# Kernel optimization log

Measured on AMD Instinct MI355X. Metric: run time of the kernel, lower is better.

Reference implementation:

```python
import jax, jax.numpy as jnp
import numpy as np

TOP_P = 0.9  # forward default arg, fixed to exercise the top-p path


def setup_inputs() -> dict:
    key = jax.random.key(0)
    k1, k2 = jax.random.split(key)
    B, V = 128, 128000
    logits = jax.random.normal(k1, (B, V), dtype=jnp.float32) * 2.0
    # temperatures in [0.5, 1.5) to avoid divide-by-near-zero
    temperatures = jax.random.uniform(k2, (B,), dtype=jnp.float32, minval=0.5, maxval=1.5)
    return {"logits": logits, "temperatures": temperatures, "top_k": 50}


def reference(logits, temperatures, top_k):
    B, V = logits.shape
    neg_inf = jnp.float32(-jnp.inf)

    # temperature scale + softmax
    scaled = logits.astype(jnp.float32) / temperatures[:, None]
    probs = jax.nn.softmax(scaled, axis=-1)  # (B, V)

    brow = jnp.arange(B)[:, None]

    # top-k filter: keep top-k probs, fill rest with -inf (matches torch scatter into full(-inf))
    if top_k > 0:
        k = min(top_k, V)
        vals, idx = jax.lax.top_k(probs, k)  # (B, k)
        probs = jnp.full_like(probs, neg_inf).at[brow, idx].set(vals)

    # top-p (nucleus) filter: sort desc, cumsum, mask tail beyond top_p (always keep first)
    if TOP_P < 1.0:
        order = jnp.argsort(-probs, axis=-1)              # descending order indices (-inf sorts last)
        sorted_probs = jnp.take_along_axis(probs, order, axis=-1)
        cum = jnp.cumsum(sorted_probs, axis=-1)
        remove = cum > TOP_P
        remove = remove.at[:, 0].set(False)
        sorted_probs = jnp.where(remove, neg_inf, sorted_probs)
        probs = probs.at[brow, order].set(sorted_probs)   # scatter back to original positions

    # Gumbel-max-style sampling: argmax(probs / Exp(1) noise), noise clamped to >= 1e-10
    kn = jax.random.fold_in(jax.random.key(0), 1)
    noise = jnp.maximum(jax.random.exponential(kn, probs.shape, dtype=jnp.float32), 1e-10)
    return jnp.argmax(probs / noise, axis=-1)  # (B,) int tokens
```

## Files before the change

kernel.cpp:

```cpp
#include <hip/hip_runtime.h>
#include <stdint.h>
#include <limits.h>

#define THREEFRY_PARTITIONABLE 1

#define NTK   512
#define NWAVE (NTK/64)
#define RCAP  4
#define NBUCK 4096
#define BPT   (NBUCK/NTK)
#define CAPS  256
#define CAPG  2048
#define CAPF  512
#define KMAX  512
#define SMAX  32

#define NT1   1024
#define CAP1  4096

#if __has_builtin(__builtin_amdgcn_exp2f)
#define FAST_EXP2(x) __builtin_amdgcn_exp2f(x)
#else
#define FAST_EXP2(x) exp2f(x)
#endif

__device__ __forceinline__ uint32_t rotl32(uint32_t v, int r) {
  return (v << r) | (v >> (32 - r));
}
__device__ __forceinline__ void tfround(uint32_t& x0, uint32_t& x1, int r) {
  x0 += x1; x1 = rotl32(x1, r); x1 ^= x0;
}
__device__ __forceinline__ void threefry2x32(uint32_t k0, uint32_t k1,
                                             uint32_t x0, uint32_t x1,
                                             uint32_t& o0, uint32_t& o1) {
  uint32_t k2 = k0 ^ k1 ^ 0x1BD11BDAu;
  x0 += k0; x1 += k1;
  tfround(x0,x1,13); tfround(x0,x1,15); tfround(x0,x1,26); tfround(x0,x1,6);
  x0 += k1; x1 += k2 + 1u;
  tfround(x0,x1,17); tfround(x0,x1,29); tfround(x0,x1,16); tfround(x0,x1,24);
  x0 += k2; x1 += k0 + 2u;
  tfround(x0,x1,13); tfround(x0,x1,15); tfround(x0,x1,26); tfround(x0,x1,6);
  x0 += k0; x1 += k1 + 3u;
  tfround(x0,x1,17); tfround(x0,x1,29); tfround(x0,x1,16); tfround(x0,x1,24);
  x0 += k1; x1 += k2 + 4u;
  tfround(x0,x1,13); tfround(x0,x1,15); tfround(x0,x1,26); tfround(x0,x1,6);
  x0 += k2; x1 += k0 + 5u;
  o0 = x0; o1 = x1;
}
__device__ __forceinline__ float jax_noise(uint32_t kn0, uint32_t kn1,
                                           unsigned long long i,
                                           unsigned long long total) {
  uint32_t o0, o1, bits;
#if THREEFRY_PARTITIONABLE
  threefry2x32(kn0, kn1, (uint32_t)(i >> 32), (uint32_t)(i & 0xFFFFFFFFull), o0, o1);
  bits = o0 ^ o1;
#else
  unsigned long long H = total >> 1;
  if (i < H) { threefry2x32(kn0, kn1, (uint32_t)i, (uint32_t)(i + H), o0, o1); bits = o0; }
  else       { threefry2x32(kn0, kn1, (uint32_t)(i - H), (uint32_t)i, o0, o1); bits = o1; }
#endif
  float u = __uint_as_float((bits >> 9) | 0x3f800000u) - 1.0f;
  float e = -log1pf(-u);
  return fmaxf(e, 1e-10f);
}
__device__ __forceinline__ uint32_t fkey(float f) {
  uint32_t u = __float_as_uint(f);
  return u ^ ((u >> 31) ? 0xFFFFFFFFu : 0x80000000u);
}
__device__ __forceinline__ float unfkey_floor(uint32_t keyT) {
  if (keyT == 0u) return -INFINITY;
  return __uint_as_float((keyT & 0x80000000u) ? (keyT ^ 0x80000000u) : ~keyT);
}
__device__ __forceinline__ int clamp_k(int k) {
  if (k < 1) k = 1;
  if (k > KMAX) k = KMAX;
  return k;
}

__device__ __forceinline__ void block_kth_bucket(uint32_t* hist, uint32_t* wtot,
                                                 int* beta_sh, int k,
                                                 int tid, int lane, int wave) {
  const int base = tid * BPT;
  uint32_t tsum = 0;
#pragma unroll
  for (int j = 0; j < BPT; j++) tsum += hist[base + j];
  uint32_t incl = tsum;
  for (int off = 1; off < 64; off <<= 1) {
    uint32_t v = __shfl_down(incl, off);
    if (lane + off < 64) incl += v;
  }
  if (lane == 0) wtot[wave] = incl;
  __syncthreads();
  uint32_t above = incl - tsum;
  for (int w = wave + 1; w < NWAVE; w++) above += wtot[w];
  if (above < (uint32_t)k && above + tsum >= (uint32_t)k) {
    uint32_t run = above;
    for (int j = BPT - 1; j >= 0; j--) {
      run += hist[base + j];
      if (run >= (uint32_t)k) { *beta_sh = base + j; break; }
    }
  }
  __syncthreads();
}

__global__ __launch_bounds__(NTK)
void sampler_stream(const float* __restrict__ logits,
                    const float* __restrict__ temps,
                    const int* __restrict__ topk_ptr,
                    float* __restrict__ msArr,
                    double* __restrict__ dsumArr,
                    int* __restrict__ cntArr,
                    float2* __restrict__ pairs,
                    int B, int V, int S, int chunk) {
  const int blk = blockIdx.x;
  const int b = blk / S, sp = blk % S;
  const int tid = threadIdx.x, lane = tid & 63, wave = tid >> 6;

  __shared__ uint32_t hist[NBUCK];
  __shared__ float wm[NWAVE];
  __shared__ double wsum[NWAVE];
  __shared__ uint32_t wtot[NWAVE];
  __shared__ int beta_sh, cnum_sh;

  if (tid == 0) { beta_sh = 0; cnum_sh = 0; }
  for (int i = tid; i < NBUCK; i += NTK) hist[i] = 0;

  const float T = temps[b];
  const float cf = (float)(1.4426950408889634 / (double)T);
  const int k = clamp_k(*topk_ptr);

  const int start = sp * chunk;
  const int end = min(start + chunk, V);
  const float* row = logits + (size_t)b * (size_t)V;
  const int n = end - start;
  const int n4 = n >> 2;
  const float4* row4 = (const float4*)(row + start);

  float4 r[RCAP];
  float tmax = -INFINITY;
  float acc0 = 0.f, acc1 = 0.f;
#pragma unroll
  for (int it = 0; it < RCAP; it++) {
    const int i = tid + it * NTK;
    if (i < n4) {
      float4 f = row4[i];
      r[it] = f;
      tmax = fmaxf(tmax, fmaxf(fmaxf(f.x, f.y), fmaxf(f.z, f.w)));
      acc0 += FAST_EXP2(f.x * cf) + FAST_EXP2(f.z * cf);
      acc1 += FAST_EXP2(f.y * cf) + FAST_EXP2(f.w * cf);
    }
  }
  for (int i = tid + RCAP * NTK; i < n4; i += NTK) {
    float4 f = row4[i];
    tmax = fmaxf(tmax, fmaxf(fmaxf(f.x, f.y), fmaxf(f.z, f.w)));
    acc0 += FAST_EXP2(f.x * cf) + FAST_EXP2(f.z * cf);
    acc1 += FAST_EXP2(f.y * cf) + FAST_EXP2(f.w * cf);
  }
  for (int v = start + n4 * 4 + tid; v < end; v += NTK) {
    float f = row[v];
    tmax = fmaxf(tmax, f);
    acc0 += FAST_EXP2(f * cf);
  }

  float bm = tmax;
  for (int off = 32; off; off >>= 1)
    bm = fmaxf(bm, __shfl_down(bm, off));
  if (lane == 0) wm[wave] = bm;

  double ds = (double)acc0 + (double)acc1;
  for (int off = 32; off; off >>= 1)
    ds += __shfl_down(ds, off);
  if (lane == 0) wsum[wave] = ds;

  if (tmax != -INFINITY) atomicAdd(&hist[fkey(tmax) >> 20], 1u);
  __syncthreads();

  float m_sp = wm[0];
#pragma unroll
  for (int w = 1; w < NWAVE; w++) m_sp = fmaxf(m_sp, wm[w]);
  if (tid == 0) {
    msArr[blk] = m_sp;
    double t = 0.0;
    for (int w = 0; w < NWAVE; w++) t += wsum[w];
    dsumArr[blk] = t;
  }

  block_kth_bucket(hist, wtot, &beta_sh, k, tid, lane, wave);

  const float fT = unfkey_floor((uint32_t)beta_sh << 20);
  float2* myp = pairs + (size_t)blk * CAPS;

  auto emit = [&](float val, int vidx) {
    if (val >= fT) {
      int pos = atomicAdd(&cnum_sh, 1);
      if (pos < CAPS) myp[pos] = make_float2(val, __int_as_float(vidx));
    }
  };

#pragma unroll
  for (int it = 0; it < RCAP; it++) {
    const int i = tid + it * NTK;
    if (i < n4) {
      float4 f = r[it];
      const int vb = start + i * 4;
      emit(f.x, vb); emit(f.y, vb + 1); emit(f.z, vb + 2); emit(f.w, vb + 3);
    }
  }
  for (int i = tid + RCAP * NTK; i < n4; i += NTK) {
    float4 f = row4[i];
    const int vb = start + i * 4;
    emit(f.x, vb); emit(f.y, vb + 1); emit(f.z, vb + 2); emit(f.w, vb + 3);
  }
  for (int v = start + n4 * 4 + tid; v < end; v += NTK) emit(row[v], v);

  __syncthreads();
  if (tid == 0) cntArr[blk] = min(cnum_sh, CAPS);
}

__global__ __launch_bounds__(NTK)
void sampler_finalize(const float* __restrict__ temps,
                      const int* __restrict__ topk_ptr,
                      const float* __restrict__ msArr,
                      const double* __restrict__ dsumArr,
                      const int* __restrict__ cntArr,
                      const float2* __restrict__ pairs,
                      int* __restrict__ out,
                      int B, int V, int S) {
  const int b = blockIdx.x;
  const int tid = threadIdx.x, lane = tid & 63, wave = tid >> 6;

  __shared__ uint32_t hist[NBUCK];
  __shared__ float gv[CAPG];
  __shared__ int   gi[CAPG];
  __shared__ float c2v[CAPF];
  __shared__ int   c2i[CAPF];
  __shared__ float c2p[CAPF];
  __shared__ float sv[KMAX];
  __shared__ int   si[KMAX];
  __shared__ float sc[KMAX];
  __shared__ int   offL[SMAX + 1];
  __shared__ int   cnL[SMAX];
  __shared__ float msL[SMAX];
  __shared__ double dsL[SMAX];
  __shared__ uint32_t wtot[NWAVE];
  __shared__ int beta_sh, cnt2_sh, L_sh;
  __shared__ float m_sh, D_sh;

  const int k = clamp_k(*topk_ptr);
  const float T = temps[b];

  if (tid == 0) { beta_sh = 0; cnt2_sh = 0; }
  if (tid < S) {
    msL[tid] = msArr[b * S + tid];
    dsL[tid] = dsumArr[b * S + tid];
    int c = cntArr[b * S + tid];
    cnL[tid] = (c < CAPS) ? c : CAPS;
  }
  for (int i = tid; i < NBUCK; i += NTK) hist[i] = 0;
  __syncthreads();

  if (tid == 0) {
    int acc = 0;
    for (int j = 0; j < S; j++) { offL[j] = acc; acc += cnL[j]; }
    offL[S] = acc;
  }

  if (wave == 1 || (NWAVE == 1 && wave == 0)) {
    float msp = (lane < S) ? msL[lane] : -INFINITY;
    float mg = msp;
    for (int off = 32; off; off >>= 1)
      mg = fmaxf(mg, __shfl_down(mg, off));
    mg = __shfl(mg, 0);
    double term = (lane < S) ? dsL[lane] : 0.0;
    for (int off = 32; off; off >>= 1)
      term += __shfl_down(term, off);
    if (lane == 0) {
      const double cd = 1.4426950408889634 / (double)T;
      D_sh = (float)(term * exp2(-(double)mg * cd));
      m_sh = mg / T;
    }
  }
  __syncthreads();

  const int TC = min(offL[S], CAPG);

  for (int t = tid; t < TC; t += NTK) {
    int j = 0;
#pragma unroll
    for (int jj = 1; jj <= SMAX; jj++)
      if (jj <= S) j += (t >= offL[jj]);
    float2 pr = pairs[(size_t)(b * S + j) * CAPS + (t - offL[j])];
    gv[t] = pr.x;
    gi[t] = __float_as_int(pr.y);
    atomicAdd(&hist[fkey(pr.x) >> 20], 1u);
  }
  __syncthreads();

  block_kth_bucket(hist, wtot, &beta_sh, k, tid, lane, wave);

  const float fT = unfkey_floor((uint32_t)beta_sh << 20);
  for (int t = tid; t < TC; t += NTK) {
    float val = gv[t];
    if (val >= fT) {
      int pos = atomicAdd(&cnt2_sh, 1);
      if (pos < CAPF) { c2v[pos] = val; c2i[pos] = gi[t]; }
    }
  }
  __syncthreads();

  const int C = min(cnt2_sh, CAPF);
  const float m = m_sh, D = D_sh;
  for (int i = tid; i < C; i += NTK)
    c2p[i] = expf(c2v[i] / T - m) / D;
  __syncthreads();

  for (int i = tid; i < C; i += NTK) {
    float pi = c2p[i];
    int   ii = c2i[i];
    int r = 0;
    for (int j = 0; j < C; j++) {
      float pj = c2p[j];
      r += (pj > pi) || (pj == pi && c2i[j] < ii);
    }
    if (r < k) { sv[r] = pi; si[r] = ii; }
  }
  __syncthreads();

  const int kk = (k < C) ? k : C;
  if (tid == 0) {
    float cum = 0.f;
    int L = 1;
    for (int j = 0; j < kk; j++) {
      cum += sv[j];
      if (j == 0) continue;
      if (cum <= 0.9f) L = j + 1; else break;
    }
    L_sh = L;
  }
  __syncthreads();

  const int L = L_sh;
  {
    uint32_t kn0, kn1;
    threefry2x32(0u, 0u, 0u, 1u, kn0, kn1);
    unsigned long long total = (unsigned long long)B * (unsigned long long)V;
    for (int j = tid; j < L; j += NTK) {
      unsigned long long flat = (unsigned long long)b * (unsigned long long)V
                              + (unsigned long long)si[j];
      sc[j] = sv[j] / jax_noise(kn0, kn1, flat, total);
    }
  }
  __syncthreads();

  if (tid == 0) {
    float bs = -1.0f;
    int   bi = INT_MAX;
    for (int j = 0; j < L; j++) {
      if (sc[j] > bs || (sc[j] == bs && si[j] < bi)) { bs = sc[j]; bi = si[j]; }
    }
    out[b] = bi;
  }
}

__global__ __launch_bounds__(NT1, 1)
void sampler_fallback(const float* __restrict__ logits,
                      const float* __restrict__ temps,
                      const int* __restrict__ topk_ptr,
                      int* __restrict__ out,
                      int B, int V) {
  const int b    = blockIdx.x;
  const int tid  = threadIdx.x;
  const int lane = tid & 63;
  const int wave = tid >> 6;

  __shared__ uint32_t hist[NBUCK];
  __shared__ float    cand_p[CAP1];
  __shared__ int      cand_i[CAP1];
  __shared__ float    wmax[16];
  __shared__ double   wsum[16];
  __shared__ float    svals[KMAX];
  __shared__ int      sidx[KMAX];
  __shared__ float    m_sh, D_sh;
  __shared__ int      beta_sh, cnum_sh, L_sh;

  const float T = temps[b];
  const float* row = logits + (size_t)b * (size_t)V;
  int k = clamp_k(*topk_ptr);
  if (k > V) k = V;

  if (tid == 0) { beta_sh = 1; cnum_sh = 0; }
  for (int i = tid; i < NBUCK; i += NT1) hist[i] = 0;
  __syncthreads();

  float t8[8];
#pragma unroll
  for (int j = 0; j < 8; j++) t8[j] = -INFINITY;
  float mymax = -INFINITY;
  for (int v = tid; v < V; v += NT1) {
    float s = row[v] / T;
    mymax = fmaxf(mymax, s);
    if (s > t8[0]) {
      t8[0] = s;
#pragma unroll
      for (int j = 1; j < 8; j++)
        if (t8[j-1] > t8[j]) { float tmp = t8[j]; t8[j] = t8[j-1]; t8[j-1] = tmp; }
    }
  }
  for (int off = 32; off > 0; off >>= 1)
    mymax = fmaxf(mymax, __shfl_down(mymax, off));
  if (lane == 0) wmax[wave] = mymax;
#pragma unroll
  for (int j = 0; j < 8; j++)
    if (t8[j] != -INFINITY) atomicAdd(&hist[fkey(t8[j]) >> 20], 1u);
  __syncthreads();
  if (tid == 0) {
    float m = -INFINITY;
    for (int w = 0; w < 16; w++) m = fmaxf(m, wmax[w]);
    m_sh = m;
  }
  if (wave == 1) {
    int base = lane * 64;
    uint32_t ssum = 0;
    for (int j = 0; j < 64; j++) ssum += hist[base + ((j + lane) & 63)];
    uint32_t incl = ssum;
    for (int off = 1; off < 64; off <<= 1) {
      uint32_t vv = __shfl_down(incl, off);
      if (lane + off < 64) incl += vv;
    }
    uint32_t higher = incl - ssum;
    if (higher < (uint32_t)k && incl >= (uint32_t)k) {
      uint32_t run = higher;
      for (int j = 63; j >= 0; j--) {
        run += hist[base + j];
        if (run >= (uint32_t)k) { beta_sh = base + j; break; }
      }
    }
  }
  __syncthreads();
  const float m = m_sh;
  const uint32_t keyT = (uint32_t)((beta_sh >= 1 ? beta_sh - 1 : 0)) << 20;
  double dsum = 0.0;
  for (int v = tid; v < V; v += NT1) {
    float s = row[v] / T;
    float e = expf(s - m);
    dsum += (double)e;
    if (fkey(s) >= keyT) {
      int pos = atomicAdd(&cnum_sh, 1);
      if (pos < CAP1) { cand_p[pos] = e; cand_i[pos] = v; }
    }
  }
  for (int off = 32; off > 0; off >>= 1)
    dsum += __shfl_down(dsum, off);
  if (lane == 0) wsum[wave] = dsum;
  __syncthreads();
  if (tid == 0) {
    double t = 0.0;
    for (int w = 0; w < 16; w++) t += wsum[w];
    D_sh = (float)t;
  }
  __syncthreads();
  const float D = D_sh;
  const int C = (cnum_sh < CAP1) ? cnum_sh : CAP1;
  for (int i = tid; i < C; i += NT1) cand_p[i] = cand_p[i] / D;
  __syncthreads();
  for (int i = tid; i < C; i += NT1) {
    float pi = cand_p[i];
    int   ii = cand_i[i];
    int r = 0;
    for (int j = 0; j < C; j++) {
      float pj = cand_p[j];
      r += (pj > pi) || (pj == pi && cand_i[j] < ii);
    }
    if (r < k) { svals[r] = pi; sidx[r] = ii; }
  }
  __syncthreads();
  if (tid == 0) {
    float cum = 0.f;
    int L = 1;
    for (int j = 0; j < k; j++) {
      cum += svals[j];
      if (j == 0) continue;
      if (cum <= 0.9f) L = j + 1; else break;
    }
    L_sh = L;
  }
  __syncthreads();
  const int L = L_sh;
  if (tid < L) {
    uint32_t kn0, kn1;
    threefry2x32(0u, 0u, 0u, 1u, kn0, kn1);
    unsigned long long total = (unsigned long long)B * (unsigned long long)V;
    unsigned long long flat = (unsigned long long)b * (unsigned long long)V
                            + (unsigned long long)sidx[tid];
    cand_p[tid] = svals[tid] / jax_noise(kn0, kn1, flat, total);
  }
  __syncthreads();
  if (tid == 0) {
    float bs = -1.0f;
    int   bi = INT_MAX;
    for (int j = 0; j < L; j++) {
      if (cand_p[j] > bs || (cand_p[j] == bs && sidx[j] < bi)) { bs = cand_p[j]; bi = sidx[j]; }
    }
    out[b] = bi;
  }
}

extern "C" void kernel_launch(void* const* d_in, const int* in_sizes, int n_in,
                              void* d_out, int out_size, void* d_ws, size_t ws_size,
                              hipStream_t stream) {
  const float* logits = (const float*)d_in[0];
  const float* temps  = (const float*)d_in[1];
  const int*   topk   = (const int*)d_in[2];
  int* out = (int*)d_out;

  int B = in_sizes[1];
  int V = in_sizes[0] / B;

  const int ELEMS = NTK * RCAP * 4;
  int S = (V + ELEMS - 1) / ELEMS;
  if (S > SMAX) S = SMAX;
  if (S < 1) S = 1;
  size_t need;
  for (;;) {
    need = (size_t)B * S * (sizeof(double) + sizeof(float) + sizeof(int))
         + (size_t)B * S * CAPS * sizeof(float2);
    if (need <= ws_size || S <= 2) break;
    S >>= 1;
  }

  if (ws_size < need || S < 2) {
    sampler_fallback<<<dim3(B), dim3(NT1), 0, stream>>>(logits, temps, topk, out, B, V);
    return;
  }

  int chunk = (((V + S - 1) / S) + 3) & ~3;

  double* dsumArr = (double*)d_ws;
  float*  msArr   = (float*)(dsumArr + (size_t)B * S);
  int*    cntArr  = (int*)(msArr + (size_t)B * S);
  float2* pairs   = (float2*)(cntArr + (size_t)B * S);

  sampler_stream<<<dim3(B * S), dim3(NTK), 0, stream>>>(
      logits, temps, topk, msArr, dsumArr, cntArr, pairs, B, V, S, chunk);
  sampler_finalize<<<dim3(B), dim3(NTK), 0, stream>>>(
      temps, topk, msArr, dsumArr, cntArr, pairs, out, B, V, S);
}
```

Baseline: 121.8 us.

## Use larger per-block chunks and re-read only from threads that can hit the threshold

The partial pass now splits each row into about four 32K-element chunks instead of sixteen 8K-element ones. This cuts the number of per-split partial results and candidate lists that the finalize kernel must merge. The register cache of loaded float4 values is dropped. The candidate-emission pass re-reads the chunk from memory, but only in threads whose local maximum reaches the top-k bucket threshold, so most threads skip the second read. The cost is fewer, longer blocks with more serial loop iterations per thread, plus a global or cache re-read for the threads that do qualify.

```diff
diff --git a/kernel.cpp b/kernel.cpp
--- a/kernel.cpp
+++ b/kernel.cpp
@@ -6,7 +6,6 @@
 
 #define NTK   512
 #define NWAVE (NTK/64)
-#define RCAP  4
 #define NBUCK 4096
 #define BPT   (NBUCK/NTK)
 #define CAPS  256
@@ -14,6 +13,7 @@
 #define CAPF  512
 #define KMAX  512
 #define SMAX  32
+#define CHUNK_TARGET 32768
 
 #define NT1   1024
 #define CAP1  4096
@@ -136,21 +136,9 @@
   const int n4 = n >> 2;
   const float4* row4 = (const float4*)(row + start);
 
-  float4 r[RCAP];
   float tmax = -INFINITY;
   float acc0 = 0.f, acc1 = 0.f;
-#pragma unroll
-  for (int it = 0; it < RCAP; it++) {
-    const int i = tid + it * NTK;
-    if (i < n4) {
-      float4 f = row4[i];
-      r[it] = f;
-      tmax = fmaxf(tmax, fmaxf(fmaxf(f.x, f.y), fmaxf(f.z, f.w)));
-      acc0 += FAST_EXP2(f.x * cf) + FAST_EXP2(f.z * cf);
-      acc1 += FAST_EXP2(f.y * cf) + FAST_EXP2(f.w * cf);
-    }
-  }
-  for (int i = tid + RCAP * NTK; i < n4; i += NTK) {
+  for (int i = tid; i < n4; i += NTK) {
     float4 f = row4[i];
     tmax = fmaxf(tmax, fmaxf(fmaxf(f.x, f.y), fmaxf(f.z, f.w)));
     acc0 += FAST_EXP2(f.x * cf) + FAST_EXP2(f.z * cf);
@@ -175,10 +163,10 @@
   if (tmax != -INFINITY) atomicAdd(&hist[fkey(tmax) >> 20], 1u);
   __syncthreads();
 
-  float m_sp = wm[0];
+  if (tid == 0) {
+    float m_sp = wm[0];
 #pragma unroll
-  for (int w = 1; w < NWAVE; w++) m_sp = fmaxf(m_sp, wm[w]);
-  if (tid == 0) {
+    for (int w = 1; w < NWAVE; w++) m_sp = fmaxf(m_sp, wm[w]);
     msArr[blk] = m_sp;
     double t = 0.0;
     for (int w = 0; w < NWAVE; w++) t += wsum[w];
@@ -190,29 +178,20 @@
   const float fT = unfkey_floor((uint32_t)beta_sh << 20);
   float2* myp = pairs + (size_t)blk * CAPS;
 
-  auto emit = [&](float val, int vidx) {
-    if (val >= fT) {
-      int pos = atomicAdd(&cnum_sh, 1);
-      if (pos < CAPS) myp[pos] = make_float2(val, __int_as_float(vidx));
-    }
-  };
-
-#pragma unroll
-  for (int it = 0; it < RCAP; it++) {
-    const int i = tid + it * NTK;
-    if (i < n4) {
-      float4 f = r[it];
+  if (tmax >= fT) {
+    for (int i = tid; i < n4; i += NTK) {
+      float4 f = row4[i];
       const int vb = start + i * 4;
-      emit(f.x, vb); emit(f.y, vb + 1); emit(f.z, vb + 2); emit(f.w, vb + 3);
-    }
-  }
-  for (int i = tid + RCAP * NTK; i < n4; i += NTK) {
-    float4 f = row4[i];
-    const int vb = start + i * 4;
-    emit(f.x, vb); emit(f.y, vb + 1); emit(f.z, vb + 2); emit(f.w, vb + 3);
-  }
-  for (int v = start + n4 * 4 + tid; v < end; v += NTK) emit(row[v], v);
-
+      if (f.x >= fT) { int p = atomicAdd(&cnum_sh, 1); if (p < CAPS) myp[p] = make_float2(f.x, __int_as_float(vb)); }
+      if (f.y >= fT) { int p = atomicAdd(&cnum_sh, 1); if (p < CAPS) myp[p] = make_float2(f.y, __int_as_float(vb + 1)); }
+      if (f.z >= fT) { int p = atomicAdd(&cnum_sh, 1); if (p < CAPS) myp[p] = make_float2(f.z, __int_as_float(vb + 2)); }
+      if (f.w >= fT) { int p = atomicAdd(&cnum_sh, 1); if (p < CAPS) myp[p] = make_float2(f.w, __int_as_float(vb + 3)); }
+    }
+    for (int v = start + n4 * 4 + tid; v < end; v += NTK) {
+      float f = row[v];
+      if (f >= fT) { int p = atomicAdd(&cnum_sh, 1); if (p < CAPS) myp[p] = make_float2(f, __int_as_float(v)); }
+    }
+  }
   __syncthreads();
   if (tid == 0) cntArr[blk] = min(cnum_sh, CAPS);
 }
@@ -516,8 +495,7 @@
   int B = in_sizes[1];
   int V = in_sizes[0] / B;
 
-  const int ELEMS = NTK * RCAP * 4;
-  int S = (V + ELEMS - 1) / ELEMS;
+  int S = (V + CHUNK_TARGET - 1) / CHUNK_TARGET;
   if (S > SMAX) S = SMAX;
   if (S < 1) S = 1;
   size_t need;
```

New measurement: 127.6 us. 4.8% more time.
